# Kernel tuning notes

Measured on AMD Instinct MI355X. Metric: run time of the kernel, lower is better.

The kernel has to match this reference:

```python
import jax, jax.numpy as jnp
import numpy as np

N_EMBD = 1024
N_HEAD = 16
HEAD_DIM = N_EMBD // N_HEAD
EPS = 1e-5


def setup_inputs() -> dict:
    key = jax.random.key(0)
    ks = jax.random.split(key, 6)
    B, S, D = 2, 2048, N_EMBD
    s = 0.02
    return {
        "x": jax.random.normal(ks[0], (B, S, D), jnp.float32),
        "ln1_g": jnp.ones((D,), jnp.float32),
        "ln1_b": jnp.zeros((D,), jnp.float32),
        "w_attn": jax.random.normal(ks[1], (D, 3 * D), jnp.float32) * s,
        "b_attn": jnp.zeros((3 * D,), jnp.float32),
        "w_attn_proj": jax.random.normal(ks[2], (D, D), jnp.float32) * s,
        "b_attn_proj": jnp.zeros((D,), jnp.float32),
        "ln2_g": jnp.ones((D,), jnp.float32),
        "ln2_b": jnp.zeros((D,), jnp.float32),
        "w_fc": jax.random.normal(ks[3], (D, 4 * D), jnp.float32) * s,
        "b_fc": jnp.zeros((4 * D,), jnp.float32),
        "w_fc_proj": jax.random.normal(ks[4], (4 * D, D), jnp.float32) * s,
        "b_fc_proj": jnp.zeros((D,), jnp.float32),
    }


def _layernorm(x, g, b):
    mu = jnp.mean(x, axis=-1, keepdims=True)
    var = jnp.mean(jnp.square(x - mu), axis=-1, keepdims=True)
    return (x - mu) * jax.lax.rsqrt(var + EPS) * g + b


def _block(x, ln1_g, ln1_b, w_attn, b_attn, w_attn_proj, b_attn_proj,
           ln2_g, ln2_b, w_fc, b_fc, w_fc_proj, b_fc_proj):
    B, S, D = x.shape
    h = _layernorm(x, ln1_g, ln1_b)
    qkv = h @ w_attn + b_attn                       # [B,S,3D]
    q, k, v = jnp.split(qkv, 3, axis=-1)
    # [B,H,S,hd]
    q = q.reshape(B, S, N_HEAD, HEAD_DIM).transpose(0, 2, 1, 3)
    k = k.reshape(B, S, N_HEAD, HEAD_DIM).transpose(0, 2, 1, 3)
    v = v.reshape(B, S, N_HEAD, HEAD_DIM).transpose(0, 2, 1, 3)
    scores = jnp.einsum("bhqd,bhkd->bhqk", q, k) / jnp.sqrt(
        jnp.asarray(HEAD_DIM, x.dtype))
    causal = jnp.tril(jnp.ones((S, S), bool))
    scores = jnp.where(causal, scores, -jnp.inf)
    attn = jax.nn.softmax(scores, axis=-1)
    out = jnp.einsum("bhqk,bhkd->bhqd", attn, v)    # [B,H,S,hd]
    out = out.transpose(0, 2, 1, 3).reshape(B, S, D)
    x = x + (out @ w_attn_proj + b_attn_proj)
    h2 = _layernorm(x, ln2_g, ln2_b)
    m = jax.nn.gelu(h2 @ w_fc + b_fc, approximate=False)
    x = x + (m @ w_fc_proj + b_fc_proj)
    return x


def reference(x, ln1_g, ln1_b, w_attn, b_attn, w_attn_proj, b_attn_proj,
              ln2_g, ln2_b, w_fc, b_fc, w_fc_proj, b_fc_proj):
    return _block(x, ln1_g, ln1_b, w_attn, b_attn, w_attn_proj, b_attn_proj,
                  ln2_g, ln2_b, w_fc, b_fc, w_fc_proj, b_fc_proj)
```

## Files before the change

kernel.cpp:

```cpp
#include <hip/hip_runtime.h>
#include <hip/hip_bf16.h>
#include <math.h>

typedef __bf16 bf16_t;
typedef bf16_t bf16x8 __attribute__((ext_vector_type(8)));
typedef float f32x4 __attribute__((ext_vector_type(4)));
typedef float f32x16 __attribute__((ext_vector_type(16)));
typedef unsigned short u16;
typedef u16 ushort8 __attribute__((ext_vector_type(8)));

static __device__ __forceinline__ u16 f2bf(float f) {
    unsigned u = __builtin_bit_cast(unsigned, f);
    u += 0x7FFFu + ((u >> 16) & 1u);
    return (u16)(u >> 16);
}
static __device__ __forceinline__ float bf2f(u16 v) {
    unsigned u = (unsigned)v << 16;
    return __builtin_bit_cast(float, u);
}

static __device__ __forceinline__ int swz_row(int s, int lane) {
    const int t = (lane & 7) ^ ((lane >> 3) & 7);
    return s * 16 + ((lane >> 3) << 1) + (t >> 2);
}
static __device__ __forceinline__ int swz_kk(int lane) {
    const int t = (lane & 7) ^ ((lane >> 3) & 7);
    return (t & 3) << 3;
}
static __device__ __forceinline__ int swz_rd(int R, int c) {
    return (R >> 1) * 64 + (((((R & 1) << 2) + c) ^ ((R >> 1) & 7)) << 3);
}

static __device__ __forceinline__ int aidx32(int R, int s, int lane) {
    return R * 64 + (((((s << 1) | (lane >> 5))) ^ (R & 7)) << 3);
}

__global__ __launch_bounds__(256) void ln_kernel(
    const float* __restrict__ x, const float* __restrict__ g,
    const float* __restrict__ be, u16* __restrict__ out)
{
    const int row = blockIdx.x;
    const int tid = threadIdx.x;
    const float4 v = ((const float4*)(x + (long)row * 1024))[tid];
    float s = v.x + v.y + v.z + v.w;
#pragma unroll
    for (int d = 32; d >= 1; d >>= 1) s += __shfl_xor(s, d);
    __shared__ float r1[4], r2[4];
    if ((tid & 63) == 0) r1[tid >> 6] = s;
    __syncthreads();
    const float mean = (r1[0] + r1[1] + r1[2] + r1[3]) * (1.0f / 1024.0f);
    const float dx = v.x - mean, dy = v.y - mean, dz = v.z - mean, dw = v.w - mean;
    float sq = dx * dx + dy * dy + dz * dz + dw * dw;
#pragma unroll
    for (int d = 32; d >= 1; d >>= 1) sq += __shfl_xor(sq, d);
    if ((tid & 63) == 0) r2[tid >> 6] = sq;
    __syncthreads();
    const float var = (r2[0] + r2[1] + r2[2] + r2[3]) * (1.0f / 1024.0f);
    const float rstd = rsqrtf(var + 1e-5f);
    const float4 gg = ((const float4*)g)[tid];
    const float4 bb = ((const float4*)be)[tid];
    ushort4 o;
    o.x = f2bf(dx * rstd * gg.x + bb.x);
    o.y = f2bf(dy * rstd * gg.y + bb.y);
    o.z = f2bf(dz * rstd * gg.z + bb.z);
    o.w = f2bf(dw * rstd * gg.w + bb.w);
    *(ushort4*)&out[(long)row * 1024 + tid * 4] = o;
}

__global__ __launch_bounds__(256) void tcvt_kernel(
    const float* __restrict__ in, u16* __restrict__ outT, int R, int C)
{
    __shared__ float tile[32][33];
    const int tx = threadIdx.x, ty = threadIdx.y;
    const int c0 = blockIdx.x * 32, r0 = blockIdx.y * 32;
#pragma unroll
    for (int i = 0; i < 4; ++i)
        tile[ty + i * 8][tx] = in[(long)(r0 + ty + i * 8) * C + c0 + tx];
    __syncthreads();
#pragma unroll
    for (int i = 0; i < 4; ++i)
        outT[(long)(c0 + ty + i * 8) * R + r0 + tx] = f2bf(tile[tx][ty + i * 8]);
}

template <int EPI>
static __device__ __forceinline__ void gemm256_body(
    const u16* __restrict__ A, const u16* __restrict__ Bt,
    const float* __restrict__ bias, const float* __restrict__ resid,
    void* __restrict__ C, int M, int N, int K)
{
    __shared__ __align__(16) u16 As[3][256 * 32];
    __shared__ __align__(16) u16 Bs[3][256 * 32];
    const int tid = threadIdx.x;
    const int lane = tid & 63;
    const int w = tid >> 6;
    const int wm = w >> 2, wn = w & 3;
    const int bm = blockIdx.x, bn = blockIdx.y;
    f32x4 acc[8][4] = {};

    const u16* Ablk = A + (long)bm * 256 * K;
    const u16* Bblk = Bt + (long)bn * 256 * K;
    const int NT = K >> 5;

    long soff[2];
#pragma unroll
    for (int i = 0; i < 2; ++i)
        soff[i] = (long)swz_row(w * 2 + i, lane) * K + swz_kk(lane);

    auto stageA = [&](int buf, int kb, int i) {
        __builtin_amdgcn_global_load_lds(
            (const __attribute__((address_space(1))) void*)(Ablk + soff[i] + kb),
            (__attribute__((address_space(3))) void*)(&As[buf][(w * 2 + i) * 512]),
            16, 0, 0);
    };
    auto stageB = [&](int buf, int kb, int i) {
        __builtin_amdgcn_global_load_lds(
            (const __attribute__((address_space(1))) void*)(Bblk + soff[i] + kb),
            (__attribute__((address_space(3))) void*)(&Bs[buf][(w * 2 + i) * 512]),
            16, 0, 0);
    };

    stageA(0, 0, 0);  stageA(0, 0, 1);  stageB(0, 0, 0);  stageB(0, 0, 1);
    stageA(1, 32, 0); stageA(1, 32, 1); stageB(1, 32, 0); stageB(1, 32, 1);

    int buf = 0;
    for (int t = 0; t < NT; ++t) {
        int nbuf = buf + 2; if (nbuf >= 3) nbuf -= 3;
        const int kb2 = (t + 2) << 5;
        const bool pf = (t + 2) < NT;
        const int c = lane >> 4;
        bf16x8 af[8], bfr[4];

        if (pf) stageA(nbuf, kb2, 0);
        if (pf)               asm volatile("s_waitcnt vmcnt(5)" ::: "memory");
        else if (t + 1 < NT)  asm volatile("s_waitcnt vmcnt(4)" ::: "memory");
        else                  asm volatile("s_waitcnt vmcnt(0)" ::: "memory");
        __builtin_amdgcn_s_barrier();
        asm volatile("" ::: "memory");
#pragma unroll
        for (int f = 0; f < 4; ++f)
            af[f] = *(const bf16x8*)&As[buf][swz_rd(wm * 128 + f * 16 + (lane & 15), c)];
#pragma unroll
        for (int n = 0; n < 2; ++n)
            bfr[n] = *(const bf16x8*)&Bs[buf][swz_rd(wn * 64 + n * 16 + (lane & 15), c)];
        __builtin_amdgcn_s_setprio(1);
#pragma unroll
        for (int f = 0; f < 4; ++f)
#pragma unroll
            for (int n = 0; n < 2; ++n)
                acc[f][n] = __builtin_amdgcn_mfma_f32_16x16x32_bf16(af[f], bfr[n], acc[f][n], 0, 0, 0);
        __builtin_amdgcn_s_setprio(0);
        asm volatile("" ::: "memory");

#pragma unroll
        for (int n = 2; n < 4; ++n)
            bfr[n] = *(const bf16x8*)&Bs[buf][swz_rd(wn * 64 + n * 16 + (lane & 15), c)];
        if (pf) stageA(nbuf, kb2, 1);
        __builtin_amdgcn_s_barrier();
        asm volatile("" ::: "memory");
        __builtin_amdgcn_s_setprio(1);
#pragma unroll
        for (int f = 0; f < 4; ++f)
#pragma unroll
            for (int n = 2; n < 4; ++n)
                acc[f][n] = __builtin_amdgcn_mfma_f32_16x16x32_bf16(af[f], bfr[n], acc[f][n], 0, 0, 0);
        __builtin_amdgcn_s_setprio(0);
        asm volatile("" ::: "memory");

#pragma unroll
        for (int f = 4; f < 8; ++f)
            af[f] = *(const bf16x8*)&As[buf][swz_rd(wm * 128 + f * 16 + (lane & 15), c)];
        if (pf) stageB(nbuf, kb2, 0);
        __builtin_amdgcn_s_barrier();
        asm volatile("" ::: "memory");
        __builtin_amdgcn_s_setprio(1);
#pragma unroll
        for (int f = 4; f < 8; ++f)
#pragma unroll
            for (int n = 0; n < 2; ++n)
                acc[f][n] = __builtin_amdgcn_mfma_f32_16x16x32_bf16(af[f], bfr[n], acc[f][n], 0, 0, 0);
        __builtin_amdgcn_s_setprio(0);
        asm volatile("" ::: "memory");

        if (pf) stageB(nbuf, kb2, 1);
        __builtin_amdgcn_s_barrier();
        asm volatile("" ::: "memory");
        __builtin_amdgcn_s_setprio(1);
#pragma unroll
        for (int f = 4; f < 8; ++f)
#pragma unroll
            for (int n = 2; n < 4; ++n)
                acc[f][n] = __builtin_amdgcn_mfma_f32_16x16x32_bf16(af[f], bfr[n], acc[f][n], 0, 0, 0);
        __builtin_amdgcn_s_setprio(0);
        asm volatile("" ::: "memory");

        buf = (buf == 2) ? 0 : buf + 1;
    }

    const int rowBase = bm * 256 + wm * 128;
    const int colBase = bn * 256 + wn * 64;
#pragma unroll
    for (int n = 0; n < 4; ++n) {
        const int col = colBase + n * 16 + (lane & 15);
        const float bv = bias[col];
#pragma unroll
        for (int m = 0; m < 8; ++m) {
#pragma unroll
            for (int r = 0; r < 4; ++r) {
                const int row = rowBase + m * 16 + (lane >> 4) * 4 + r;
                float v = acc[m][n][r] + bv;
                if constexpr (EPI == 1) {
                    const float u = v + 0.044715f * v * v * v;
                    v = v / (1.0f + __expf(-1.5957691216057308f * u));
                }
                if constexpr (EPI == 3) {
                    if (col < 1024) v *= 0.125f;
                }
                ((u16*)C)[(long)row * N + col] = f2bf(v);
            }
        }
    }
}

__global__ __launch_bounds__(512, 2) void gemm_qkv(
    const u16* A, const u16* Bt, const float* bias, const float* resid,
    void* C, int M, int N, int K) { gemm256_body<3>(A, Bt, bias, resid, C, M, N, K); }
__global__ __launch_bounds__(512, 2) void gemm_fc(
    const u16* A, const u16* Bt, const float* bias, const float* resid,
    void* C, int M, int N, int K) { gemm256_body<1>(A, Bt, bias, resid, C, M, N, K); }

template <int EPI, int DP>
static __device__ __forceinline__ void gemm128_body(
    const u16* __restrict__ A, const u16* __restrict__ Bt,
    const float* __restrict__ bias, const float* __restrict__ resid,
    void* __restrict__ C, int M, int N, int Kloop, int ldA)
{
    constexpr int MR = 4, NR = 4;
    constexpr int LPW = 4;
    __shared__ __align__(16) u16 As[DP][128 * 32];
    __shared__ __align__(16) u16 Bs[DP][128 * 32];
    const int tid = threadIdx.x;
    const int lane = tid & 63;
    const int w = tid >> 6;
    const int wm = w >> 1, wn = w & 1;
    const int bm = blockIdx.x, bn = blockIdx.y;
    f32x4 acc[MR][NR] = {};

    const u16* Ablk = A + (long)bm * 128 * ldA;
    const u16* Bblk = Bt + (long)bn * 128 * ldA;
    const int nt = Kloop >> 5;

    long soff[2];
#pragma unroll
    for (int i = 0; i < 2; ++i)
        soff[i] = (long)swz_row(w * 2 + i, lane) * ldA + swz_kk(lane);

    auto stage = [&](int buf, int kb) {
#pragma unroll
        for (int i = 0; i < 2; ++i) {
            __builtin_amdgcn_global_load_lds(
                (const __attribute__((address_space(1))) void*)(Ablk + soff[i] + kb),
                (__attribute__((address_space(3))) void*)(&As[buf][(w * 2 + i) * 512]),
                16, 0, 0);
            __builtin_amdgcn_global_load_lds(
                (const __attribute__((address_space(1))) void*)(Bblk + soff[i] + kb),
                (__attribute__((address_space(3))) void*)(&Bs[buf][(w * 2 + i) * 512]),
                16, 0, 0);
        }
    };

#pragma unroll
    for (int s = 0; s < DP - 1; ++s) stage(s, s << 5);

    for (int t = 0; t < nt; ++t) {
        const int cur = t % DP;
        if (t + DP - 2 < nt) {
            asm volatile("s_waitcnt vmcnt(%0)" :: "i"((DP - 2) * LPW) : "memory");
        } else if (t + 1 < nt) {
            asm volatile("s_waitcnt vmcnt(%0)" :: "i"(LPW) : "memory");
        } else {
            asm volatile("s_waitcnt vmcnt(0)" ::: "memory");
        }
        __builtin_amdgcn_s_barrier();
        asm volatile("" ::: "memory");

        if (t + DP - 1 < nt) stage((t + DP - 1) % DP, (t + DP - 1) << 5);

        bf16x8 af[MR], bfr[NR];
        const int c = lane >> 4;
#pragma unroll
        for (int m = 0; m < MR; ++m)
            af[m] = *(const bf16x8*)&As[cur][swz_rd(wm * 64 + m * 16 + (lane & 15), c)];
#pragma unroll
        for (int n = 0; n < NR; ++n)
            bfr[n] = *(const bf16x8*)&Bs[cur][swz_rd(wn * 64 + n * 16 + (lane & 15), c)];
#pragma unroll
        for (int m = 0; m < MR; ++m)
#pragma unroll
            for (int n = 0; n < NR; ++n)
                acc[m][n] = __builtin_amdgcn_mfma_f32_16x16x32_bf16(af[m], bfr[n], acc[m][n], 0, 0, 0);
        asm volatile("" ::: "memory");
    }

    const int rowBase = bm * 128 + wm * 64;
    const int colBase = bn * 128 + wn * 64;
#pragma unroll
    for (int n = 0; n < NR; ++n) {
        const int col = colBase + n * 16 + (lane & 15);
        const float bv = bias ? bias[col] : 0.0f;
#pragma unroll
        for (int m = 0; m < MR; ++m) {
#pragma unroll
            for (int r = 0; r < 4; ++r) {
                const int row = rowBase + m * 16 + (lane >> 4) * 4 + r;
                float v = acc[m][n][r] + bv;
                if constexpr (EPI == 2) {
                    ((float*)C)[(long)row * N + col] = v + resid[(long)row * N + col];
                } else {
                    ((u16*)C)[(long)row * N + col] = f2bf(v);
                }
            }
        }
    }
}

template <int EPI>
static __device__ __forceinline__ void gemm64w32_body(
    const u16* __restrict__ A, const u16* __restrict__ Bt,
    const float* __restrict__ bias, const float* __restrict__ resid,
    void* __restrict__ C, int M, int N, int K)
{
    __shared__ __align__(16) u16 As[2][64 * 64];
    const int tid = threadIdx.x;
    const int lane = tid & 63;
    const int w = tid >> 6;
    const int bm = blockIdx.x, bn = blockIdx.y;
    f32x16 acc[2] = {};

    const u16* Ablk = A + (long)bm * 64 * K;
    const u16* Bblk = Bt + (long)bn * 128 * K;
    const int nt = K >> 6;

    const u16* bpB = Bblk + (long)(w * 32 + (lane & 31)) * K + ((lane >> 5) << 3);

    long soffA[2];
#pragma unroll
    for (int i = 0; i < 2; ++i)
        soffA[i] = (long)((w * 2 + i) * 8 + (lane >> 3)) * K
                 + (((lane & 7) ^ (lane >> 3)) << 3);

    auto stageA = [&](int buf, int kb) {
#pragma unroll
        for (int i = 0; i < 2; ++i)
            __builtin_amdgcn_global_load_lds(
                (const __attribute__((address_space(1))) void*)(Ablk + soffA[i] + kb),
                (__attribute__((address_space(3))) void*)(&As[buf][(w * 2 + i) * 512]),
                16, 0, 0);
    };

    ushort8 Ba[4], Bb[4];
    stageA(0, 0);
    __builtin_amdgcn_sched_barrier(0);
    asm volatile("global_load_dwordx4 %0, %1, off" : "=v"(Ba[0]) : "v"(bpB));
    asm volatile("global_load_dwordx4 %0, %1, off" : "=v"(Ba[1]) : "v"(bpB + 16));
    asm volatile("global_load_dwordx4 %0, %1, off" : "=v"(Ba[2]) : "v"(bpB + 32));
    asm volatile("global_load_dwordx4 %0, %1, off" : "=v"(Ba[3]) : "v"(bpB + 48));

    auto iter = [&](int t, ushort8 (&cur)[4], ushort8 (&pf)[4]) {
        asm volatile("s_waitcnt vmcnt(4)" ::: "memory");
        __builtin_amdgcn_s_barrier();
        asm volatile("" ::: "memory");
        const bool more = (t + 1 < nt);
        if (more) {
            stageA((t + 1) & 1, (t + 1) << 6);
            __builtin_amdgcn_sched_barrier(0);
            const u16* p = bpB + ((long)(t + 1) << 6);
            asm volatile("global_load_dwordx4 %0, %1, off" : "=v"(pf[0]) : "v"(p));
            asm volatile("global_load_dwordx4 %0, %1, off" : "=v"(pf[1]) : "v"(p + 16));
            asm volatile("global_load_dwordx4 %0, %1, off" : "=v"(pf[2]) : "v"(p + 32));
            asm volatile("global_load_dwordx4 %0, %1, off" : "=v"(pf[3]) : "v"(p + 48));
        }
        bf16x8 af[2][4];
#pragma unroll
        for (int m = 0; m < 2; ++m)
#pragma unroll
            for (int s = 0; s < 4; ++s)
                af[m][s] = *(const bf16x8*)&As[t & 1][aidx32(m * 32 + (lane & 31), s, lane)];
        if (more) asm volatile("s_waitcnt vmcnt(6)" ::: "memory");
        else      asm volatile("s_waitcnt vmcnt(0)" ::: "memory");
        __builtin_amdgcn_sched_barrier(0);
        bf16x8 b[4];
#pragma unroll
        for (int i = 0; i < 4; ++i) b[i] = __builtin_bit_cast(bf16x8, cur[i]);
#pragma unroll
        for (int s = 0; s < 4; ++s)
#pragma unroll
            for (int m = 0; m < 2; ++m)
                acc[m] = __builtin_amdgcn_mfma_f32_32x32x16_bf16(af[m][s], b[s], acc[m], 0, 0, 0);
        asm volatile("" ::: "memory");
    };

    for (int t = 0; t < nt; t += 2) {
        iter(t, Ba, Bb);
        iter(t + 1, Bb, Ba);
    }

    const int rowBase = bm * 64;
    const int col = bn * 128 + w * 32 + (lane & 31);
    const float bv = bias[col];
#pragma unroll
    for (int m = 0; m < 2; ++m) {
#pragma unroll
        for (int reg = 0; reg < 16; ++reg) {
            const int row = rowBase + m * 32 + (reg & 3) + 8 * (reg >> 2) + 4 * (lane >> 5);
            float v = acc[m][reg] + bv;
            if constexpr (EPI == 2) {
                ((float*)C)[(long)row * N + col] = v + resid[(long)row * N + col];
            } else {
                ((u16*)C)[(long)row * N + col] = f2bf(v);
            }
        }
    }
}

__global__ __launch_bounds__(256) void gemm_ap(
    const u16* A, const u16* Bt, const float* bias, const float* resid,
    void* C, int M, int N, int K) { gemm64w32_body<2>(A, Bt, bias, resid, C, M, N, K); }

__global__ __launch_bounds__(256) void gemm_fp_part(
    const u16* A, const u16* Bt, u16* P, int M, int N, int Kfull)
{
    const int kh = blockIdx.z;
    gemm128_body<0, 3>(A + kh * 2048, Bt + kh * 2048, nullptr, nullptr,
                       P + (size_t)kh * 4096 * 1024, M, N, 2048, Kfull);
}

__global__ __launch_bounds__(256) void reduce_fp(
    const u16* __restrict__ p0, const u16* __restrict__ p1,
    const float* __restrict__ bias, float* __restrict__ out)
{
    const long e = ((long)blockIdx.x * 256 + threadIdx.x) * 8;
    const int col = (int)(e & 1023);
    const ushort8 a = *(const ushort8*)&p0[e];
    const ushort8 b = *(const ushort8*)&p1[e];
    const float4 bi0 = *(const float4*)&bias[col];
    const float4 bi1 = *(const float4*)&bias[col + 4];
    float4 r0 = *(const float4*)&out[e];
    float4 r1 = *(const float4*)&out[e + 4];
    r0.x += bf2f(a[0]) + bf2f(b[0]) + bi0.x;
    r0.y += bf2f(a[1]) + bf2f(b[1]) + bi0.y;
    r0.z += bf2f(a[2]) + bf2f(b[2]) + bi0.z;
    r0.w += bf2f(a[3]) + bf2f(b[3]) + bi0.w;
    r1.x += bf2f(a[4]) + bf2f(b[4]) + bi1.x;
    r1.y += bf2f(a[5]) + bf2f(b[5]) + bi1.y;
    r1.z += bf2f(a[6]) + bf2f(b[6]) + bi1.z;
    r1.w += bf2f(a[7]) + bf2f(b[7]) + bi1.w;
    *(float4*)&out[e] = r0;
    *(float4*)&out[e + 4] = r1;
}

__global__ __launch_bounds__(256) void attn_kernel(
    const u16* __restrict__ qkv, u16* __restrict__ outb)
{
    const int S = 2048;
    const int flat = blockIdx.x + 16 * blockIdx.y;
    const int work = (flat & 7) * 64 + (flat >> 3);
    const int ipair = work & 15;
    const int bh = work >> 4;
    const int b = bh >> 4, h = bh & 15;
    const int tid = threadIdx.x, lane = tid & 63, w = tid >> 6;
    __shared__ __align__(16) u16 Ks[2][64 * 72];
    __shared__ __align__(16) u16 Vs[2][64 * 72];
    __shared__ __align__(16) u16 Ps[4][16 * 72];

    const long base = (long)b * S * 3072;
    const int rstage = tid >> 3;
    const int cg = (tid & 7) * 8;
    const int sw = cg;
    const u16* kbase = qkv + base + 1024 + h * 64 + cg;
    const u16* vbase = qkv + base + 2048 + h * 64 + cg;

    for (int half = 0; half < 2; ++half) {
        const int qt = half ? 31 - ipair : ipair;
        const int q0 = qt * 64;

        bf16x8 qf[2];
        {
            const int qrow = q0 + w * 16 + (lane & 15);
#pragma unroll
            for (int c = 0; c < 2; ++c)
                qf[c] = *(const bf16x8*)&qkv[base + (long)qrow * 3072 + h * 64 + c * 32 + (lane >> 4) * 8];
        }

        f32x4 Of[4] = {};
        float m = -1e30f, l = 0.0f;

        ushort8 kr[2], vr[2];
#pragma unroll
        for (int it = 0; it < 2; ++it) {
            const long ro = (long)(it * 32 + rstage) * 3072;
            kr[it] = *(const ushort8*)&kbase[ro];
            vr[it] = *(const ushort8*)&vbase[ro];
        }
        __syncthreads();
#pragma unroll
        for (int it = 0; it < 2; ++it) {
            const int r = it * 32 + rstage;
            *(ushort8*)&Ks[0][r * 72 + cg] = kr[it];
#pragma unroll
            for (int j = 0; j < 8; ++j)
                Vs[0][(cg + j) * 72 + (r ^ sw)] = vr[it][j];
        }

        for (int kt = 0; kt <= qt; ++kt) {
            const int cur = kt & 1;
            if (kt < qt) {
#pragma unroll
                for (int it = 0; it < 2; ++it) {
                    const long ro = (long)((kt + 1) * 64 + it * 32 + rstage) * 3072;
                    kr[it] = *(const ushort8*)&kbase[ro];
                    vr[it] = *(const ushort8*)&vbase[ro];
                }
            }
            __syncthreads();

            f32x4 Sf[4] = {};
            __builtin_amdgcn_s_setprio(1);
#pragma unroll
            for (int f = 0; f < 4; ++f) {
#pragma unroll
                for (int c = 0; c < 2; ++c) {
                    const bf16x8 kf = *(const bf16x8*)&Ks[cur][(f * 16 + (lane & 15)) * 72 + c * 32 + (lane >> 4) * 8];
                    Sf[f] = __builtin_amdgcn_mfma_f32_16x16x32_bf16(kf, qf[c], Sf[f], 0, 0, 0);
                }
            }
            __builtin_amdgcn_s_setprio(0);
            if (kt == qt) {
                const int ql = w * 16 + (lane & 15);
#pragma unroll
                for (int f = 0; f < 4; ++f) {
#pragma unroll
                    for (int r = 0; r < 4; ++r) {
                        const int kvl = f * 16 + ((lane >> 4) << 2) + r;
                        if (kvl > ql) Sf[f][r] = -1e30f;
                    }
                }
            }
            float pmax = Sf[0][0];
#pragma unroll
            for (int f = 0; f < 4; ++f)
#pragma unroll
                for (int r = 0; r < 4; ++r) pmax = fmaxf(pmax, Sf[f][r]);
            if (!__all(pmax <= m + 8.0f)) {
                float pm = pmax;
                pm = fmaxf(pm, __shfl_xor(pm, 16));
                pm = fmaxf(pm, __shfl_xor(pm, 32));
                const float mnew = fmaxf(m, pm);
                const float sc = __expf(m - mnew);
                m = mnew;
                l *= sc;
                float sco[4];
#pragma unroll
                for (int r = 0; r < 4; ++r)
                    sco[r] = __shfl(sc, ((lane >> 4) << 2) + r);
#pragma unroll
                for (int f = 0; f < 4; ++f)
#pragma unroll
                    for (int r = 0; r < 4; ++r) Of[f][r] *= sco[r];
            }
            float osum = 0.0f;
#pragma unroll
            for (int f = 0; f < 4; ++f)
#pragma unroll
                for (int r = 0; r < 4; ++r) {
                    const float e = __expf(Sf[f][r] - m);
                    Sf[f][r] = e;
                    osum += e;
                }
            l += osum;
#pragma unroll
            for (int f = 0; f < 4; ++f) {
                const unsigned lo = (unsigned)f2bf(Sf[f][0]) | ((unsigned)f2bf(Sf[f][1]) << 16);
                const unsigned hi = (unsigned)f2bf(Sf[f][2]) | ((unsigned)f2bf(Sf[f][3]) << 16);
                uint2 pk; pk.x = lo; pk.y = hi;
                *(uint2*)&Ps[w][(lane & 15) * 72 + f * 16 + ((lane >> 4) << 2)] = pk;
            }
            __builtin_amdgcn_s_setprio(1);
#pragma unroll
            for (int f = 0; f < 4; ++f) {
                const int hd = f * 16 + (lane & 15);
#pragma unroll
                for (int c = 0; c < 2; ++c) {
                    const int k0 = c * 32 + (lane >> 4) * 8;
                    const bf16x8 pa = *(const bf16x8*)&Ps[w][(lane & 15) * 72 + k0];
                    const bf16x8 vb = *(const bf16x8*)&Vs[cur][hd * 72 + (k0 ^ (hd & 56))];
                    Of[f] = __builtin_amdgcn_mfma_f32_16x16x32_bf16(pa, vb, Of[f], 0, 0, 0);
                }
            }
            __builtin_amdgcn_s_setprio(0);
            if (kt < qt) {
#pragma unroll
                for (int it = 0; it < 2; ++it) {
                    const int r = it * 32 + rstage;
                    *(ushort8*)&Ks[cur ^ 1][r * 72 + cg] = kr[it];
#pragma unroll
                    for (int j = 0; j < 8; ++j)
                        Vs[cur ^ 1][(cg + j) * 72 + (r ^ sw)] = vr[it][j];
                }
            }
        }

        float lt = l;
        lt += __shfl_xor(lt, 16);
        lt += __shfl_xor(lt, 32);
        const float linv = 1.0f / lt;
        float inv[4];
#pragma unroll
        for (int r = 0; r < 4; ++r)
            inv[r] = __shfl(linv, ((lane >> 4) << 2) + r);
#pragma unroll
        for (int f = 0; f < 4; ++f) {
            const int col = h * 64 + f * 16 + (lane & 15);
#pragma unroll
            for (int r = 0; r < 4; ++r) {
                const int qrow = q0 + w * 16 + (lane >> 4) * 4 + r;
                outb[((long)b * S + qrow) * 1024 + col] = f2bf(Of[f][r] * inv[r]);
            }
        }
    }
}

extern "C" void kernel_launch(void* const* d_in, const int* in_sizes, int n_in,
                              void* d_out, int out_size, void* d_ws, size_t ws_size,
                              hipStream_t stream) {
    const float* x      = (const float*)d_in[0];
    const float* ln1_g  = (const float*)d_in[1];
    const float* ln1_b  = (const float*)d_in[2];
    const float* w_attn = (const float*)d_in[3];
    const float* b_attn = (const float*)d_in[4];
    const float* w_ap   = (const float*)d_in[5];
    const float* b_ap   = (const float*)d_in[6];
    const float* ln2_g  = (const float*)d_in[7];
    const float* ln2_b  = (const float*)d_in[8];
    const float* w_fc   = (const float*)d_in[9];
    const float* b_fc   = (const float*)d_in[10];
    const float* w_fp   = (const float*)d_in[11];
    const float* b_fp   = (const float*)d_in[12];
    float* out = (float*)d_out;

    const int R = 4096;
    char* p = (char*)d_ws;
    u16*   wTa  = (u16*)(p);
    u16*   wTap = (u16*)(p + 6291456);
    u16*   wTfc = (u16*)(p + 8388608);
    u16*   wTfp = (u16*)(p + 16777216);
    u16*   hao  = (u16*)(p + 25165824);
    u16*   qkv  = (u16*)(p + 33554432);
    u16*   mb   = hao;
    u16*   h2   = wTa;
    u16*   fpp  = (u16*)(p);
    float* x1   = out;

    const dim3 tb(32, 8);
    tcvt_kernel<<<dim3(3072 / 32, 1024 / 32), tb, 0, stream>>>(w_attn, wTa, 1024, 3072);
    tcvt_kernel<<<dim3(1024 / 32, 1024 / 32), tb, 0, stream>>>(w_ap, wTap, 1024, 1024);
    tcvt_kernel<<<dim3(4096 / 32, 1024 / 32), tb, 0, stream>>>(w_fc, wTfc, 1024, 4096);
    tcvt_kernel<<<dim3(1024 / 32, 4096 / 32), tb, 0, stream>>>(w_fp, wTfp, 4096, 1024);

    ln_kernel<<<R, 256, 0, stream>>>(x, ln1_g, ln1_b, hao);
    gemm_qkv<<<dim3(16, 12), 512, 0, stream>>>(hao, wTa, b_attn, nullptr, qkv, R, 3072, 1024);
    attn_kernel<<<dim3(16, 32), 256, 0, stream>>>(qkv, hao);
    gemm_ap<<<dim3(64, 8), 256, 0, stream>>>(hao, wTap, b_ap, x, x1, R, 1024, 1024);
    ln_kernel<<<R, 256, 0, stream>>>(x1, ln2_g, ln2_b, h2);
    gemm_fc<<<dim3(16, 16), 512, 0, stream>>>(h2, wTfc, b_fc, nullptr, mb, R, 4096, 1024);
    gemm_fp_part<<<dim3(32, 8, 2), 256, 0, stream>>>(mb, wTfp, fpp, R, 1024, 4096);
    reduce_fp<<<2048, 256, 0, stream>>>(fpp, fpp + (size_t)4096 * 1024, b_fp, out);
}
```

Measured before the change: 263.9 us.

## Retile QKV GEMM to 128x128 and rewrite split-K FC-proj with direct B loads

Moves the QKV projection from the 256x256 512-thread GEMM to the 128x128 256-thread kernel, launching four times as many blocks so more CUs have work. Rewrites the split-K FC projection GEMM as a 64x128 tile kernel. In that kernel A is staged to LDS via global_load_lds in a triple buffer, B fragments go straight into registers, and waits are hand-scheduled with vmcnt. This gives more blocks and finer-grained pipelining, at the cost of less operand reuse per block and fragile manual wait counts.

After: 262.8 us. No clear change (-0.4%).

```diff
diff --git a/kernel.cpp b/kernel.cpp
--- a/kernel.cpp
+++ b/kernel.cpp
@@ -212,18 +212,12 @@
                     const float u = v + 0.044715f * v * v * v;
                     v = v / (1.0f + __expf(-1.5957691216057308f * u));
                 }
-                if constexpr (EPI == 3) {
-                    if (col < 1024) v *= 0.125f;
-                }
                 ((u16*)C)[(long)row * N + col] = f2bf(v);
             }
         }
     }
 }
 
-__global__ __launch_bounds__(512, 2) void gemm_qkv(
-    const u16* A, const u16* Bt, const float* bias, const float* resid,
-    void* C, int M, int N, int K) { gemm256_body<3>(A, Bt, bias, resid, C, M, N, K); }
 __global__ __launch_bounds__(512, 2) void gemm_fc(
     const u16* A, const u16* Bt, const float* bias, const float* resid,
     void* C, int M, int N, int K) { gemm256_body<1>(A, Bt, bias, resid, C, M, N, K); }
@@ -313,6 +307,9 @@
             for (int r = 0; r < 4; ++r) {
                 const int row = rowBase + m * 16 + (lane >> 4) * 4 + r;
                 float v = acc[m][n][r] + bv;
+                if constexpr (EPI == 3) {
+                    if (col < 1024) v *= 0.125f;
+                }
                 if constexpr (EPI == 2) {
                     ((float*)C)[(long)row * N + col] = v + resid[(long)row * N + col];
                 } else {
@@ -322,6 +319,10 @@
         }
     }
 }
+
+__global__ __launch_bounds__(256) void gemm_qkv(
+    const u16* A, const u16* Bt, const float* bias, const float* resid,
+    void* C, int M, int N, int K) { gemm128_body<3, 3>(A, Bt, bias, resid, C, M, N, K, K); }
 
 template <int EPI>
 static __device__ __forceinline__ void gemm64w32_body(
@@ -427,11 +428,103 @@
     void* C, int M, int N, int K) { gemm64w32_body<2>(A, Bt, bias, resid, C, M, N, K); }
 
 __global__ __launch_bounds__(256) void gemm_fp_part(
-    const u16* A, const u16* Bt, u16* P, int M, int N, int Kfull)
+    const u16* __restrict__ A, const u16* __restrict__ Bt,
+    u16* __restrict__ P, int M, int N, int Kfull)
 {
+    constexpr int MR = 4, NR = 2;
+    __shared__ __align__(16) u16 As[3][64 * 32];
+    const int tid = threadIdx.x;
+    const int lane = tid & 63;
+    const int w = tid >> 6;
+    const int bm = blockIdx.x, bn = blockIdx.y;
     const int kh = blockIdx.z;
-    gemm128_body<0, 3>(A + kh * 2048, Bt + kh * 2048, nullptr, nullptr,
-                       P + (size_t)kh * 4096 * 1024, M, N, 2048, Kfull);
+    f32x4 acc[MR][NR] = {};
+
+    const int Kh = Kfull >> 1;
+    const u16* Ablk = A + (long)bm * 64 * Kfull + kh * Kh;
+    const u16* Bblk = Bt + (long)bn * 128 * Kfull + kh * Kh;
+    const int nt = Kh >> 5;
+
+    const u16* bp0 = Bblk + (long)(w * 32 + (lane & 15)) * Kfull + (lane >> 4) * 8;
+    const u16* bp1 = bp0 + 16 * Kfull;
+    const long soff = (long)swz_row(w, lane) * Kfull + swz_kk(lane);
+
+    auto stageA = [&](int buf, int kb) {
+        __builtin_amdgcn_global_load_lds(
+            (const __attribute__((address_space(1))) void*)(Ablk + soff + kb),
+            (__attribute__((address_space(3))) void*)(&As[buf][w * 512]),
+            16, 0, 0);
+    };
+
+    ushort8 B0[2], B1[2], B2[2];
+    stageA(0, 0);
+    __builtin_amdgcn_sched_barrier(0);
+    asm volatile("global_load_dwordx4 %0, %1, off" : "=v"(B0[0]) : "v"(bp0));
+    asm volatile("global_load_dwordx4 %0, %1, off" : "=v"(B0[1]) : "v"(bp1));
+    __builtin_amdgcn_sched_barrier(0);
+    stageA(1, 32);
+    __builtin_amdgcn_sched_barrier(0);
+    {
+        const u16* a0 = bp0 + 32;
+        const u16* a1 = bp1 + 32;
+        asm volatile("global_load_dwordx4 %0, %1, off" : "=v"(B1[0]) : "v"(a0));
+        asm volatile("global_load_dwordx4 %0, %1, off" : "=v"(B1[1]) : "v"(a1));
+    }
+
+    auto iter = [&](int t, int cb, int pb, ushort8 (&cur)[2], ushort8 (&pf)[2]) {
+        if (t + 1 < nt) asm volatile("s_waitcnt vmcnt(5)" ::: "memory");
+        else            asm volatile("s_waitcnt vmcnt(2)" ::: "memory");
+        __builtin_amdgcn_s_barrier();
+        asm volatile("" ::: "memory");
+        if (t + 2 < nt) {
+            stageA(pb, (t + 2) << 5);
+            __builtin_amdgcn_sched_barrier(0);
+            const u16* a0 = bp0 + ((t + 2) << 5);
+            const u16* a1 = bp1 + ((t + 2) << 5);
+            asm volatile("global_load_dwordx4 %0, %1, off" : "=v"(pf[0]) : "v"(a0));
+            asm volatile("global_load_dwordx4 %0, %1, off" : "=v"(pf[1]) : "v"(a1));
+        }
+        bf16x8 af[MR];
+        const int c = lane >> 4;
+#pragma unroll
+        for (int m = 0; m < MR; ++m)
+            af[m] = *(const bf16x8*)&As[cb][swz_rd(m * 16 + (lane & 15), c)];
+        if (t + 2 < nt)      asm volatile("s_waitcnt vmcnt(6)" ::: "memory");
+        else if (t + 1 < nt) asm volatile("s_waitcnt vmcnt(3)" ::: "memory");
+        else                 asm volatile("s_waitcnt vmcnt(0)" ::: "memory");
+        __builtin_amdgcn_sched_barrier(0);
+        const bf16x8 b0 = __builtin_bit_cast(bf16x8, cur[0]);
+        const bf16x8 b1 = __builtin_bit_cast(bf16x8, cur[1]);
+#pragma unroll
+        for (int m = 0; m < MR; ++m) {
+            acc[m][0] = __builtin_amdgcn_mfma_f32_16x16x32_bf16(af[m], b0, acc[m][0], 0, 0, 0);
+            acc[m][1] = __builtin_amdgcn_mfma_f32_16x16x32_bf16(af[m], b1, acc[m][1], 0, 0, 0);
+        }
+        asm volatile("" ::: "memory");
+    };
+
+    for (int t = 0; t + 2 < nt; t += 3) {
+        iter(t,     0, 2, B0, B2);
+        iter(t + 1, 1, 0, B1, B0);
+        iter(t + 2, 2, 1, B2, B1);
+    }
+    iter(nt - 1, 0, 2, B0, B2);
+
+    u16* Pc = P + (size_t)kh * 4096 * 1024;
+    const int rowBase = bm * 64;
+    const int colBase = bn * 128 + w * 32;
+#pragma unroll
+    for (int n = 0; n < NR; ++n) {
+        const int col = colBase + n * 16 + (lane & 15);
+#pragma unroll
+        for (int m = 0; m < MR; ++m) {
+#pragma unroll
+            for (int r = 0; r < 4; ++r) {
+                const int row = rowBase + m * 16 + (lane >> 4) * 4 + r;
+                Pc[(long)row * N + col] = f2bf(acc[m][n][r]);
+            }
+        }
+    }
 }
 
 __global__ __launch_bounds__(256) void reduce_fp(
@@ -667,11 +760,11 @@
     tcvt_kernel<<<dim3(1024 / 32, 4096 / 32), tb, 0, stream>>>(w_fp, wTfp, 4096, 1024);
 
     ln_kernel<<<R, 256, 0, stream>>>(x, ln1_g, ln1_b, hao);
-    gemm_qkv<<<dim3(16, 12), 512, 0, stream>>>(hao, wTa, b_attn, nullptr, qkv, R, 3072, 1024);
+    gemm_qkv<<<dim3(32, 24), 256, 0, stream>>>(hao, wTa, b_attn, nullptr, qkv, R, 3072, 1024);
     attn_kernel<<<dim3(16, 32), 256, 0, stream>>>(qkv, hao);
     gemm_ap<<<dim3(64, 8), 256, 0, stream>>>(hao, wTap, b_ap, x, x1, R, 1024, 1024);
     ln_kernel<<<R, 256, 0, stream>>>(x1, ln2_g, ln2_b, h2);
     gemm_fc<<<dim3(16, 16), 512, 0, stream>>>(h2, wTfc, b_fc, nullptr, mb, R, 4096, 1024);
-    gemm_fp_part<<<dim3(32, 8, 2), 256, 0, stream>>>(mb, wTfp, fpp, R, 1024, 4096);
+    gemm_fp_part<<<dim3(64, 8, 2), 256, 0, stream>>>(mb, wTfp, fpp, R, 1024, 4096);
     reduce_fp<<<2048, 256, 0, stream>>>(fpp, fpp + (size_t)4096 * 1024, b_fp, out);
 }
```
